# Optimization experiments

Measured on AMD Instinct MI355X. Metric: run time of the kernel, lower is better.

Reference implementation:

```python
import jax, jax.numpy as jnp
import numpy as np

EPS = 1e-4

@jax.custom_vjp
def binarize(x):
    # BinaryConnectDeterministic: sign with sign(0)=+1
    return jnp.where(x >= 0, 1.0, -1.0).astype(x.dtype)

def _bin_fwd(x):
    return binarize(x), x

def _bin_bwd(x, g):
    # straight-through estimator, clipped to |x| <= 1
    return (g * (jnp.abs(x) <= 1).astype(g.dtype),)

binarize.defvjp(_bin_fwd, _bin_bwd)

def ap2(x):
    # approximate power-of-2: sign(x) * 2^round(log2|x|); grad is 0 a.e. (round/sign)
    a = jnp.maximum(jnp.abs(x), 1e-38)
    return jnp.sign(x) * jnp.exp2(jnp.round(jnp.log2(a)))

def shift_bn(x, gamma, beta, axes):
    # shift-based batch norm (BNN paper): var approximated via centered*AP2(centered),
    # inverse std and gamma replaced by their AP2 approximations. Training-mode batch stats.
    mean = jnp.mean(x, axis=axes, keepdims=True)
    c = x - mean
    var = jnp.mean(c * ap2(c), axis=axes, keepdims=True)
    xhat = c * ap2(1.0 / jnp.sqrt(var + EPS))
    shape = [1] * x.ndim
    shape[1] = x.shape[1]
    return ap2(gamma.reshape(shape)) * xhat + beta.reshape(shape)

def conv_bin(x, w, b):
    y = jax.lax.conv_general_dilated(x, binarize(w), (1, 1), [(1, 1), (1, 1)],
                                     dimension_numbers=('NCHW', 'OIHW', 'NCHW'))
    return y + b[None, :, None, None]

def maxpool3s2(x):
    return jax.lax.reduce_window(x, -jnp.inf, jax.lax.max,
                                 (1, 1, 3, 3), (1, 1, 2, 2), 'VALID')


def setup_inputs() -> dict:
    key = jax.random.key(0)
    ks = jax.random.split(key, 8)
    B, NU = 2048, 2048
    inp = {
        'x': jax.random.normal(ks[0], (B, 784), jnp.float32),
        'conv1_w': jax.random.normal(ks[1], (32, 1, 3, 3), jnp.float32) * 0.1,
        'conv1_b': jnp.zeros((32,), jnp.float32),
        'g1': jnp.ones((32,), jnp.float32), 'b1': jnp.zeros((32,), jnp.float32),
        'conv2_w': jax.random.normal(ks[2], (64, 32, 3, 3), jnp.float32) * 0.1,
        'conv2_b': jnp.zeros((64,), jnp.float32),
        'g2': jnp.ones((64,), jnp.float32), 'b2': jnp.zeros((64,), jnp.float32),
        'lin3_w': jax.random.normal(ks[3], (NU, 10816), jnp.float32) * 0.02,
        'lin3_b': jnp.zeros((NU,), jnp.float32),
        'g3': jnp.ones((NU,), jnp.float32), 'b3': jnp.zeros((NU,), jnp.float32),
        'lin4_w': jax.random.normal(ks[4], (10, NU), jnp.float32) * 0.02,
        'lin4_b': jnp.zeros((10,), jnp.float32),
    }
    return inp


def reference(x, conv1_w, conv1_b, g1, b1, conv2_w, conv2_b, g2, b2,
              lin3_w, lin3_b, g3, b3, lin4_w, lin4_b):
    h = x.reshape(-1, 1, 28, 28)
    h = jax.nn.relu(conv_bin(h, conv1_w, conv1_b))
    h = shift_bn(h, g1, b1, axes=(0, 2, 3))
    h = binarize(h)
    h = jax.nn.relu(conv_bin(h, conv2_w, conv2_b))
    h = maxpool3s2(h)                       # [B,64,13,13]
    h = shift_bn(h, g2, b2, axes=(0, 2, 3))
    h = binarize(h)
    h = h.reshape(h.shape[0], -1)           # [B,10816]
    h = jax.nn.relu(h @ binarize(lin3_w).T + lin3_b)
    h = shift_bn(h, g3, b3, axes=(0,))
    h = binarize(h)
    return h @ binarize(lin4_w).T + lin4_b  # [B,10] (no norm4/logsoftmax in forward)
```

## Files before the change

### kernel.cpp

```cpp
#include <hip/hip_runtime.h>

#define BB 2048
#define IMG 784
#define HWD 28
#define C1 32
#define C2 64
#define PP 169
#define PD 13
#define F3 10816
#define N3 2048
#define K3W 169
#define K3P 176
#define K4W 32
#define NOUT 10
#define CONV 27
#define PADW 30
#define OCCHUNK 8
#define OCH 32
#define SCRS 736

typedef unsigned long long u64;

__device__ __forceinline__ float ap2mag(float c) {
    unsigned int a = __float_as_uint(c) & 0x7fffffffu;
    unsigned int e = (a >> 23) + ((a & 0x7fffffu) > 0x3504f3u);
    return __uint_as_float(e << 23);
}
__device__ __forceinline__ float ap2sgn(float g) {
    unsigned int u = __float_as_uint(g);
    unsigned int a = u & 0x7fffffffu;
    if (a == 0) return 0.f;
    unsigned int e = (a >> 23) + ((a & 0x7fffffu) > 0x3504f3u);
    return __uint_as_float((u & 0x80000000u) | (e << 23));
}

__global__ __launch_bounds__(256) void stage0(const float* __restrict__ x,
                                              const float* __restrict__ w1, const float* __restrict__ cb1,
                                              float* __restrict__ part1, float* __restrict__ w1b,
                                              const float* __restrict__ w2, unsigned int* __restrict__ w2p,
                                              const float* __restrict__ w3, u64* __restrict__ wp3,
                                              const float* __restrict__ w4, u64* __restrict__ wp4) {
    __shared__ float xs[30 * PADW];
    __shared__ float red[4 * C1];
    int n = blockIdx.x, tid = threadIdx.x;
    int lane = tid & 63, wv = tid >> 6;
    {
        int wid = (n * 256 + tid) >> 6;
        int nw = (gridDim.x * 256) >> 6;
        for (int w = wid; w < N3 * K3P; w += nw) {
            int nn = w / K3P, j = w - nn * K3P;
            u64 mask = 0;
            if (j < K3W) {
                float wvl = w3[(size_t)nn * F3 + j * 64 + lane];
                mask = __ballot(wvl >= 0.f);
            }
            if (lane == 0) wp3[w] = mask;
        }
    }
    if (n == 0) {
        for (int i = tid; i < C1 * 9; i += 256) w1b[i] = (w1[i] >= 0.f) ? 1.f : -1.f;
    } else if (n == 1) {
        for (int t = tid; t < C2 * 9; t += 256) {
            int oc = t / 9, k = t % 9;
            unsigned int bits = 0;
            for (int ic = 0; ic < C1; ic++)
                bits |= (w2[oc * 288 + ic * 9 + k] >= 0.f ? 1u : 0u) << ic;
            w2p[t] = bits;
        }
    } else if (n == 2) {
        for (int w = wv; w < NOUT * K4W; w += 4) {
            int o = w / K4W, j = w % K4W;
            float wvl = w4[o * N3 + j * 64 + lane];
            u64 mask = __ballot(wvl >= 0.f);
            if (lane == 0) wp4[w] = mask;
        }
    }
    for (int i = tid; i < 30 * PADW; i += 256) {
        int r = i / PADW - 1, c = i % PADW - 1;
        float v = 0.f;
        if (r >= 0 && r < HWD && c >= 0 && c < HWD) v = x[n * IMG + r * HWD + c];
        xs[i] = v;
    }
    __syncthreads();
    bool act = tid < 196;
    int r = tid / 7, c0 = (tid % 7) * 4;
    float win[18];
#pragma unroll
    for (int k = 0; k < 18; k++) win[k] = 0.f;
    if (act) {
#pragma unroll
        for (int ry = 0; ry < 3; ry++)
#pragma unroll
            for (int cx = 0; cx < 6; cx++)
                win[ry * 6 + cx] = xs[(r + ry) * PADW + c0 + cx];
    }
#pragma unroll
    for (int ch = 0; ch < C1; ch++) {
        float a = 0.f;
        if (act) {
            float k0 = (w1[ch * 9 + 0] >= 0.f) ? 1.f : -1.f, k1 = (w1[ch * 9 + 1] >= 0.f) ? 1.f : -1.f;
            float k2 = (w1[ch * 9 + 2] >= 0.f) ? 1.f : -1.f, k3 = (w1[ch * 9 + 3] >= 0.f) ? 1.f : -1.f;
            float k4 = (w1[ch * 9 + 4] >= 0.f) ? 1.f : -1.f, k5 = (w1[ch * 9 + 5] >= 0.f) ? 1.f : -1.f;
            float k6 = (w1[ch * 9 + 6] >= 0.f) ? 1.f : -1.f, k7 = (w1[ch * 9 + 7] >= 0.f) ? 1.f : -1.f;
            float k8 = (w1[ch * 9 + 8] >= 0.f) ? 1.f : -1.f;
            float b = cb1[ch];
#pragma unroll
            for (int px = 0; px < 4; px++) {
                float s = win[px] * k0 + win[px + 1] * k1 + win[px + 2] * k2
                        + win[6 + px] * k3 + win[7 + px] * k4 + win[8 + px] * k5
                        + win[12 + px] * k6 + win[13 + px] * k7 + win[14 + px] * k8;
                a += fmaxf(s + b, 0.f);
            }
        }
        for (int off = 32; off; off >>= 1) a += __shfl_down(a, off);
        if (lane == 0) red[wv * C1 + ch] = a;
    }
    __syncthreads();
    if (tid < C1) part1[n * C1 + tid] = red[tid] + red[C1 + tid] + red[2 * C1 + tid] + red[3 * C1 + tid];
}

__global__ __launch_bounds__(256) void conv1_var(const float* __restrict__ x,
                            const float* __restrict__ w1b,
                            const float* __restrict__ cb1, const float* __restrict__ mean1,
                            float* __restrict__ part) {
    __shared__ float xs[30 * PADW];
    __shared__ float red[4 * C1];
    int n = blockIdx.x, tid = threadIdx.x;
    for (int i = tid; i < 30 * PADW; i += 256) {
        int r = i / PADW - 1, c = i % PADW - 1;
        float v = 0.f;
        if (r >= 0 && r < HWD && c >= 0 && c < HWD) v = x[n * IMG + r * HWD + c];
        xs[i] = v;
    }
    __syncthreads();
    bool act = tid < 196;
    int r = tid / 7, c0 = (tid % 7) * 4;
    float win[18];
#pragma unroll
    for (int k = 0; k < 18; k++) win[k] = 0.f;
    if (act) {
#pragma unroll
        for (int ry = 0; ry < 3; ry++)
#pragma unroll
            for (int cx = 0; cx < 6; cx++)
                win[ry * 6 + cx] = xs[(r + ry) * PADW + c0 + cx];
    }
    int lane = tid & 63, wv = tid >> 6;
#pragma unroll
    for (int ch = 0; ch < C1; ch++) {
        float a = 0.f;
        if (act) {
            float k0 = w1b[ch * 9 + 0], k1 = w1b[ch * 9 + 1], k2 = w1b[ch * 9 + 2];
            float k3 = w1b[ch * 9 + 3], k4 = w1b[ch * 9 + 4], k5 = w1b[ch * 9 + 5];
            float k6 = w1b[ch * 9 + 6], k7 = w1b[ch * 9 + 7], k8 = w1b[ch * 9 + 8];
            float b = cb1[ch], m = mean1[ch];
#pragma unroll
            for (int px = 0; px < 4; px++) {
                float s = win[px] * k0 + win[px + 1] * k1 + win[px + 2] * k2
                        + win[6 + px] * k3 + win[7 + px] * k4 + win[8 + px] * k5
                        + win[12 + px] * k6 + win[13 + px] * k7 + win[14 + px] * k8;
                float v = fmaxf(s + b, 0.f);
                float c = v - m;
                a += fabsf(c) * ap2mag(c);
            }
        }
        for (int off = 32; off; off >>= 1) a += __shfl_down(a, off);
        if (lane == 0) red[wv * C1 + ch] = a;
    }
    __syncthreads();
    if (tid < C1) part[n * C1 + tid] = red[tid] + red[C1 + tid] + red[2 * C1 + tid] + red[3 * C1 + tid];
}

__global__ __launch_bounds__(256) void conv1_pack(const float* __restrict__ x,
                           const float* __restrict__ w1b,
                           const float* __restrict__ cb1, const float* __restrict__ mean1,
                           const float* __restrict__ scale1, const float* __restrict__ beta1,
                           unsigned int* __restrict__ s1p) {
    __shared__ float xs[30 * PADW];
    int n = blockIdx.x, tid = threadIdx.x;
    for (int i = tid; i < 30 * PADW; i += 256) {
        int r = i / PADW - 1, c = i % PADW - 1;
        float v = 0.f;
        if (r >= 0 && r < HWD && c >= 0 && c < HWD) v = x[n * IMG + r * HWD + c];
        xs[i] = v;
    }
    __syncthreads();
    if (tid >= 196) return;
    int r = tid / 7, c0 = (tid % 7) * 4;
    float win[18];
#pragma unroll
    for (int ry = 0; ry < 3; ry++)
#pragma unroll
        for (int cx = 0; cx < 6; cx++)
            win[ry * 6 + cx] = xs[(r + ry) * PADW + c0 + cx];
    unsigned int bits0 = 0, bits1 = 0, bits2 = 0, bits3 = 0;
#pragma unroll
    for (int ch = 0; ch < C1; ch++) {
        float k0 = w1b[ch * 9 + 0], k1 = w1b[ch * 9 + 1], k2 = w1b[ch * 9 + 2];
        float k3 = w1b[ch * 9 + 3], k4 = w1b[ch * 9 + 4], k5 = w1b[ch * 9 + 5];
        float k6 = w1b[ch * 9 + 6], k7 = w1b[ch * 9 + 7], k8 = w1b[ch * 9 + 8];
        float b = cb1[ch], m = mean1[ch], sc = scale1[ch], bt = beta1[ch];
#pragma unroll
        for (int px = 0; px < 4; px++) {
            float s = win[px] * k0 + win[px + 1] * k1 + win[px + 2] * k2
                    + win[6 + px] * k3 + win[7 + px] * k4 + win[8 + px] * k5
                    + win[12 + px] * k6 + win[13 + px] * k7 + win[14 + px] * k8;
            float v = fmaxf(s + b, 0.f);
            float val = sc * (v - m) + bt;
            unsigned int bit = (val >= 0.f ? 1u : 0u) << ch;
            if (px == 0) bits0 |= bit;
            else if (px == 1) bits1 |= bit;
            else if (px == 2) bits2 |= bit;
            else bits3 |= bit;
        }
    }
    uint4 w4v = make_uint4(bits0, bits1, bits2, bits3);
    *reinterpret_cast<uint4*>(&s1p[n * IMG + r * HWD + c0]) = w4v;
}

__global__ __launch_bounds__(256) void conv2pool(const unsigned int* __restrict__ s1p,
                                                 const unsigned int* __restrict__ w2p,
                                                 const float* __restrict__ cb2,
                                                 short* __restrict__ p2i,
                                                 float* __restrict__ part2) {
    __shared__ unsigned int spad[29 * PADW];
    __shared__ short scr[OCCHUNK * SCRS];
    __shared__ float psum[OCCHUNK * PP];
    __shared__ float pm[OCH];
    int n = blockIdx.x, ocb = blockIdx.y * OCH, tid = threadIdx.x;
    for (int i = tid; i < 29 * PADW; i += 256) {
        int r = i / PADW, c = i - r * PADW;
        unsigned int v = 0;
        if (r >= 1 && c >= 1 && c <= 28) v = s1p[n * IMG + (r - 1) * HWD + (c - 1)];
        spad[i] = v;
    }
    __syncthreads();
    unsigned int win[3][9];
    bool top_[3], left_[3];
    bool act2 = (tid + 512) < CONV * CONV;
#pragma unroll
    for (int pi = 0; pi < 3; pi++) {
        int p = tid + pi * 256;
        if (p >= CONV * CONV) p = 0;
        int y = p / CONV, xx = p - y * CONV;
        top_[pi] = (y == 0);
        left_[pi] = (xx == 0);
        const unsigned int* bp = &spad[y * PADW + xx];
#pragma unroll
        for (int ky = 0; ky < 3; ky++)
#pragma unroll
            for (int kx = 0; kx < 3; kx++)
                win[pi][ky * 3 + kx] = bp[ky * PADW + kx];
    }
    int lane = tid & 63, wv = tid >> 6;
    for (int base = 0; base < OCH; base += OCCHUNK) {
        for (int ol = 0; ol < OCCHUNK; ol++) {
            int oc = ocb + base + ol;
            unsigned int w0 = w2p[oc * 9 + 0], w1 = w2p[oc * 9 + 1], w2 = w2p[oc * 9 + 2];
            unsigned int w3 = w2p[oc * 9 + 3], w4 = w2p[oc * 9 + 4], w5 = w2p[oc * 9 + 5];
            unsigned int w6 = w2p[oc * 9 + 6], w7 = w2p[oc * 9 + 7], w8 = w2p[oc * 9 + 8];
            int p0 = __popc(w0), p1 = __popc(w1), p2 = __popc(w2);
            int p3 = __popc(w3), p6 = __popc(w6);
            int ct = 192 + 2 * (p0 + p1 + p2);
            int cl = 192 + 2 * (p0 + p3 + p6);
            int cc = 128 + 2 * (p0 + p1 + p2 + p3 + p6);
#pragma unroll
            for (int pi = 0; pi < 3; pi++) {
                int s = __popc(win[pi][0] ^ w0) + __popc(win[pi][1] ^ w1) + __popc(win[pi][2] ^ w2)
                      + __popc(win[pi][3] ^ w3) + __popc(win[pi][4] ^ w4) + __popc(win[pi][5] ^ w5)
                      + __popc(win[pi][6] ^ w6) + __popc(win[pi][7] ^ w7) + __popc(win[pi][8] ^ w8);
                int off = top_[pi] ? (left_[pi] ? cc : ct) : (left_[pi] ? cl : 288);
                if (pi < 2 || act2) scr[ol * SCRS + tid + pi * 256] = (short)(off - 2 * s);
            }
        }
        __syncthreads();
        for (int q = tid; q < OCCHUNK * PP; q += 256) {
            int ol = q / PP, pix = q - ol * PP;
            int py = pix / PD, px = pix - py * PD;
            const short* rr = &scr[ol * SCRS + (2 * py) * CONV + 2 * px];
            int m0 = max(max((int)rr[0], (int)rr[1]), (int)rr[2]);
            int m1 = max(max((int)rr[CONV], (int)rr[CONV + 1]), (int)rr[CONV + 2]);
            int m2 = max(max((int)rr[2 * CONV], (int)rr[2 * CONV + 1]), (int)rr[2 * CONV + 2]);
            int val = max(max(m0, m1), m2);
            p2i[n * F3 + (ocb + base + ol) * PP + pix] = (short)val;
            psum[q] = fmaxf((float)val + cb2[ocb + base + ol], 0.f);
        }
        __syncthreads();
        for (int ol = wv; ol < OCCHUNK; ol += 4) {
            float a = 0.f;
            for (int p = lane; p < PP; p += 64) a += psum[ol * PP + p];
            for (int off = 32; off; off >>= 1) a += __shfl_down(a, off);
            if (lane == 0) pm[base + ol] = a;
        }
        __syncthreads();
    }
    if (tid < OCH) part2[n * C2 + ocb + tid] = pm[tid];
}

__global__ __launch_bounds__(256) void p2_var(const short* __restrict__ p2i,
                         const float* __restrict__ cb2,
                         const float* __restrict__ mean2, float* __restrict__ part) {
    int n = blockIdx.x, tid = threadIdx.x, lane = tid & 63, wv = tid >> 6;
    const short* rowb = p2i + (size_t)n * F3;
    __shared__ float red[C2];
#pragma unroll
    for (int i = 0; i < 16; i++) {
        int ch = wv * 16 + i;
        const short* row = rowb + ch * PP;
        float b = cb2[ch];
        float m = mean2[ch];
        float a = 0.f;
        for (int p = lane; p < PP; p += 64) {
            float v = fmaxf((float)row[p] + b, 0.f);
            float c = v - m;
            a += fabsf(c) * ap2mag(c);
        }
        for (int off = 32; off; off >>= 1) a += __shfl_down(a, off);
        if (lane == 0) red[ch] = a;
    }
    __syncthreads();
    if (tid < C2) part[n * C2 + tid] = red[tid];
}

__global__ __launch_bounds__(256) void reduce_stats(const float* __restrict__ part, int nch, int nblk,
                             const float* __restrict__ g, float* __restrict__ outv,
                             int mode, double count) {
    int ch = blockIdx.x, tid = threadIdx.x;
    double a = 0.0;
    for (int i = tid; i < nblk; i += 256) a += (double)part[(size_t)i * nch + ch];
    __shared__ double red[4];
    for (int off = 32; off; off >>= 1) a += __shfl_down(a, off);
    int lane = tid & 63, wv = tid >> 6;
    if (lane == 0) red[wv] = a;
    __syncthreads();
    if (tid == 0) {
        double s = red[0] + red[1] + red[2] + red[3];
        if (mode == 0) {
            outv[ch] = (float)(s / count);
        } else {
            float var = (float)(s / count);
            float inv = 1.0f / sqrtf(var + 1e-4f);
            outv[ch] = ap2sgn(g[ch]) * ap2mag(inv);
        }
    }
}

__global__ void p2_pack(const short* __restrict__ p2i, const float* __restrict__ cb2,
                        const float* __restrict__ mean2, const float* __restrict__ scale2,
                        const float* __restrict__ beta2, u64* __restrict__ hp3) {
    int lane = threadIdx.x & 63;
    int wid = (blockIdx.x * blockDim.x + threadIdx.x) >> 6;
    int nw = (gridDim.x * blockDim.x) >> 6;
    for (int w = wid; w < BB * K3P; w += nw) {
        int n = w / K3P, j = w - n * K3P;
        u64 mask = 0;
        if (j < K3W) {
            int f = j * 64 + lane;
            int oc = f / PP;
            float v = fmaxf((float)p2i[n * F3 + f] + cb2[oc], 0.f);
            float val = scale2[oc] * (v - mean2[oc]) + beta2[oc];
            mask = __ballot(val >= 0.f);
        }
        if (lane == 0) hp3[w] = mask;
    }
}

__global__ __launch_bounds__(256) void lin3_gemm(const u64* __restrict__ hp3,
                                                 const u64* __restrict__ wp3,
                                                 const float* __restrict__ b3l,
                                                 float* __restrict__ h3,
                                                 float* __restrict__ part3) {
    __shared__ u64 aT[8][128];
    __shared__ u64 bT[8][64];
    __shared__ float csr[4][64];
    int tid = threadIdx.x;
    int tx = tid & 15, ty = tid >> 4;
    int m0 = blockIdx.y * 128, n0 = blockIdx.x * 64;
    int arow = tid >> 1, akk = (tid & 1) * 4;
    int bcol = tid >> 2, bkk = (tid & 3) * 2;
    const u64* aps = &hp3[(size_t)(m0 + arow) * K3P + akk];
    const u64* bps = &wp3[(size_t)(n0 + bcol) * K3P + bkk];
    int s[8][4];
#pragma unroll
    for (int i = 0; i < 8; i++)
#pragma unroll
        for (int j = 0; j < 4; j++) s[i][j] = 0;
    for (int k0 = 0; k0 < K3P; k0 += 8) {
        u64 a0 = aps[0], a1 = aps[1], a2 = aps[2], a3 = aps[3];
        u64 b0 = bps[0], b1 = bps[1];
        aps += 8; bps += 8;
        aT[akk + 0][arow] = a0; aT[akk + 1][arow] = a1;
        aT[akk + 2][arow] = a2; aT[akk + 3][arow] = a3;
        bT[bkk + 0][bcol] = b0; bT[bkk + 1][bcol] = b1;
        __syncthreads();
#pragma unroll
        for (int kk = 0; kk < 8; kk++) {
            u64 b[4], a[8];
#pragma unroll
            for (int j = 0; j < 4; j++) b[j] = bT[kk][j * 16 + tx];
#pragma unroll
            for (int i = 0; i < 8; i++) a[i] = aT[kk][i * 16 + ty];
#pragma unroll
            for (int i = 0; i < 8; i++)
#pragma unroll
                for (int j = 0; j < 4; j++) s[i][j] += (int)__popcll(a[i] ^ b[j]);
        }
        __syncthreads();
    }
    float cs[4] = {0.f, 0.f, 0.f, 0.f};
#pragma unroll
    for (int i = 0; i < 8; i++) {
        int m = m0 + i * 16 + ty;
#pragma unroll
        for (int j = 0; j < 4; j++) {
            int nn = n0 + j * 16 + tx;
            float v = fmaxf((float)(F3 - 2 * s[i][j]) + b3l[nn], 0.f);
            h3[(size_t)m * N3 + nn] = v;
            cs[j] += v;
        }
    }
    int lane = tid & 63, wv = tid >> 6;
#pragma unroll
    for (int j = 0; j < 4; j++) {
        cs[j] += __shfl_xor(cs[j], 16);
        cs[j] += __shfl_xor(cs[j], 32);
        if (lane < 16) csr[wv][j * 16 + lane] = cs[j];
    }
    __syncthreads();
    if (tid < 64)
        part3[(size_t)blockIdx.y * N3 + n0 + tid] =
            csr[0][tid] + csr[1][tid] + csr[2][tid] + csr[3][tid];
}

__global__ __launch_bounds__(256) void h3_finish(const float* __restrict__ h3,
                                                 const float* __restrict__ part3,
                                                 const float* __restrict__ g3,
                                                 float* __restrict__ mean3, float* __restrict__ scale3) {
    int nn = blockIdx.x, tid = threadIdx.x;
    __shared__ float msh;
    __shared__ double redd[4];
    if (tid < 64) {
        float a = (tid < 16) ? part3[(size_t)tid * N3 + nn] : 0.f;
        for (int off = 8; off; off >>= 1) a += __shfl_down(a, off);
        if (tid == 0) { float m = a / (float)BB; mean3[nn] = m; msh = m; }
    }
    __syncthreads();
    float m = msh;
    float acc = 0.f;
#pragma unroll
    for (int q = 0; q < 8; q++) {
        float v = h3[(size_t)(q * 256 + tid) * N3 + nn];
        float c = v - m;
        acc += fabsf(c) * ap2mag(c);
    }
    double a = (double)acc;
    for (int off = 32; off; off >>= 1) a += __shfl_down(a, off);
    int lane = tid & 63, wv = tid >> 6;
    if (lane == 0) redd[wv] = a;
    __syncthreads();
    if (tid == 0) {
        float var = (float)((redd[0] + redd[1] + redd[2] + redd[3]) / (double)BB);
        float inv = 1.0f / sqrtf(var + 1e-4f);
        scale3[nn] = ap2sgn(g3[nn]) * ap2mag(inv);
    }
}

__global__ __launch_bounds__(256) void h4_out(const float* __restrict__ h3,
                                              const float* __restrict__ mean3, const float* __restrict__ scale3,
                                              const float* __restrict__ bt3,
                                              const u64* __restrict__ wp4, const float* __restrict__ b4,
                                              float* __restrict__ out) {
    __shared__ u64 hb[K4W];
    __shared__ u64 wsh[NOUT * 33];
    int m = blockIdx.x, tid = threadIdx.x, lane = tid & 63, wv = tid >> 6;
    for (int i = tid; i < NOUT * K4W; i += 256) wsh[(i / K4W) * 33 + (i % K4W)] = wp4[i];
#pragma unroll
    for (int q = 0; q < 8; q++) {
        int j = wv * 8 + q;
        int f = j * 64 + lane;
        float v = h3[(size_t)m * N3 + f];
        float val = scale3[f] * (v - mean3[f]) + bt3[f];
        u64 mask = __ballot(val >= 0.f);
        if (lane == 0) hb[j] = mask;
    }
    __syncthreads();
    if (tid < NOUT) {
        int c = 0;
#pragma unroll
        for (int k = 0; k < K4W; k++) c += (int)__popcll(hb[k] ^ wsh[tid * 33 + k]);
        out[m * NOUT + tid] = (float)(N3 - 2 * c) + b4[tid];
    }
}

extern "C" void kernel_launch(void* const* d_in, const int* in_sizes, int n_in,
                              void* d_out, int out_size, void* d_ws, size_t ws_size,
                              hipStream_t stream) {
    const float* x   = (const float*)d_in[0];
    const float* w1  = (const float*)d_in[1];
    const float* cb1 = (const float*)d_in[2];
    const float* g1  = (const float*)d_in[3];
    const float* bt1 = (const float*)d_in[4];
    const float* w2  = (const float*)d_in[5];
    const float* cb2 = (const float*)d_in[6];
    const float* g2  = (const float*)d_in[7];
    const float* bt2 = (const float*)d_in[8];
    const float* w3  = (const float*)d_in[9];
    const float* b3l = (const float*)d_in[10];
    const float* g3  = (const float*)d_in[11];
    const float* bt3 = (const float*)d_in[12];
    const float* w4  = (const float*)d_in[13];
    const float* b4l = (const float*)d_in[14];
    float* out = (float*)d_out;

    char* base = (char*)d_ws;
    size_t off = 0;
    auto carve = [&](size_t bytes) { char* p = base + off; off = (off + bytes + 255) & ~(size_t)255; return p; };
    unsigned int* s1p  = (unsigned int*)carve((size_t)BB * IMG * 4);
    short* p2i         = (short*)carve((size_t)BB * C2 * PP * 2);
    u64* hp3           = (u64*)carve((size_t)BB * K3P * 8);
    u64* wp3           = (u64*)carve((size_t)N3 * K3P * 8);
    float* h3          = (float*)carve((size_t)BB * N3 * 4);
    u64* wp4           = (u64*)carve((size_t)NOUT * K4W * 8);
    unsigned int* w2p  = (unsigned int*)carve((size_t)C2 * 9 * 4);
    float* w1b         = (float*)carve((size_t)C1 * 9 * 4);
    float* part1       = (float*)carve((size_t)BB * C1 * 4);
    float* part2       = (float*)carve((size_t)BB * C2 * 4);
    float* part3       = (float*)carve((size_t)16 * N3 * 4);
    float* fstats      = (float*)carve((size_t)(32 + 32 + 64 + 64 + 2048 + 2048) * 4);
    float* mean1 = fstats;          float* scale1 = fstats + 32;
    float* mean2 = fstats + 64;     float* scale2 = fstats + 128;
    float* mean3 = fstats + 192;    float* scale3 = fstats + 2240;

    stage0<<<BB, 256, 0, stream>>>(x, w1, cb1, part1, w1b, w2, w2p, w3, wp3, w4, wp4);
    reduce_stats<<<C1, 256, 0, stream>>>(part1, C1, BB, g1, mean1, 0, (double)BB * IMG);
    conv1_var<<<BB, 256, 0, stream>>>(x, w1b, cb1, mean1, part1);
    reduce_stats<<<C1, 256, 0, stream>>>(part1, C1, BB, g1, scale1, 1, (double)BB * IMG);
    conv1_pack<<<BB, 256, 0, stream>>>(x, w1b, cb1, mean1, scale1, bt1, s1p);
    conv2pool<<<dim3(BB, 2), 256, 0, stream>>>(s1p, w2p, cb2, p2i, part2);
    reduce_stats<<<C2, 256, 0, stream>>>(part2, C2, BB, g2, mean2, 0, (double)BB * PP);
    p2_var<<<BB, 256, 0, stream>>>(p2i, cb2, mean2, part2);
    reduce_stats<<<C2, 256, 0, stream>>>(part2, C2, BB, g2, scale2, 1, (double)BB * PP);
    p2_pack<<<1024, 256, 0, stream>>>(p2i, cb2, mean2, scale2, bt2, hp3);
    lin3_gemm<<<dim3(32, 16), 256, 0, stream>>>(hp3, wp3, b3l, h3, part3);
    h3_finish<<<N3, 256, 0, stream>>>(h3, part3, g3, mean3, scale3);
    h4_out<<<BB, 256, 0, stream>>>(h3, mean3, scale3, bt3, wp4, b4l, out);

    (void)in_sizes; (void)n_in; (void)out_size; (void)ws_size;
}
```

Before: 624.9 us.

## Replace XOR-popcount lin3 GEMM with int8 MFMA on ±1 bytes

Lin3 inputs and weights are now stored as int8 ±1 bytes instead of packed bit words, and the GEMM uses the 16x16x64 int8 MFMA instruction with 128x128 block tiles and register prefetch of the next K chunk. This replaces the scalar popcount ALU loop with matrix-core throughput. In exchange the operand memory traffic grows eightfold (about 22 MB for the weights and 22 MB for activations), and the workspace buffers are aliased to fit, which depends on buffer lifetimes not overlapping.

```diff
diff --git a/kernel.cpp b/kernel.cpp
--- a/kernel.cpp
+++ b/kernel.cpp
@@ -9,8 +9,6 @@
 #define PD 13
 #define F3 10816
 #define N3 2048
-#define K3W 169
-#define K3P 176
 #define K4W 32
 #define NOUT 10
 #define CONV 27
@@ -20,6 +18,7 @@
 #define SCRS 736
 
 typedef unsigned long long u64;
+typedef int v4i __attribute__((ext_vector_type(4)));
 
 __device__ __forceinline__ float ap2mag(float c) {
     unsigned int a = __float_as_uint(c) & 0x7fffffffu;
@@ -38,23 +37,23 @@
                                               const float* __restrict__ w1, const float* __restrict__ cb1,
                                               float* __restrict__ part1, float* __restrict__ w1b,
                                               const float* __restrict__ w2, unsigned int* __restrict__ w2p,
-                                              const float* __restrict__ w3, u64* __restrict__ wp3,
+                                              const float* __restrict__ w3, char* __restrict__ wp3i,
                                               const float* __restrict__ w4, u64* __restrict__ wp4) {
     __shared__ float xs[30 * PADW];
     __shared__ float red[4 * C1];
     int n = blockIdx.x, tid = threadIdx.x;
     int lane = tid & 63, wv = tid >> 6;
     {
-        int wid = (n * 256 + tid) >> 6;
-        int nw = (gridDim.x * 256) >> 6;
-        for (int w = wid; w < N3 * K3P; w += nw) {
-            int nn = w / K3P, j = w - nn * K3P;
-            u64 mask = 0;
-            if (j < K3W) {
-                float wvl = w3[(size_t)nn * F3 + j * 64 + lane];
-                mask = __ballot(wvl >= 0.f);
-            }
-            if (lane == 0) wp3[w] = mask;
+        int idx = n * 256 + tid;
+        int nthr = gridDim.x * 256;
+        int total = (N3 * F3) / 4;
+        for (int t = idx; t < total; t += nthr) {
+            float4 wv4 = *(const float4*)(w3 + (size_t)t * 4);
+            unsigned int w = (wv4.x >= 0.f ? 0x01u : 0xffu)
+                           | (wv4.y >= 0.f ? 0x01u : 0xffu) << 8
+                           | (wv4.z >= 0.f ? 0x01u : 0xffu) << 16
+                           | (wv4.w >= 0.f ? 0x01u : 0xffu) << 24;
+            *(unsigned int*)(wp3i + (size_t)t * 4) = w;
         }
     }
     if (n == 0) {
@@ -345,91 +344,100 @@
     }
 }
 
-__global__ void p2_pack(const short* __restrict__ p2i, const float* __restrict__ cb2,
+__global__ __launch_bounds__(256) void p2_packi8(const short* __restrict__ p2i, const float* __restrict__ cb2,
                         const float* __restrict__ mean2, const float* __restrict__ scale2,
-                        const float* __restrict__ beta2, u64* __restrict__ hp3) {
-    int lane = threadIdx.x & 63;
-    int wid = (blockIdx.x * blockDim.x + threadIdx.x) >> 6;
-    int nw = (gridDim.x * blockDim.x) >> 6;
-    for (int w = wid; w < BB * K3P; w += nw) {
-        int n = w / K3P, j = w - n * K3P;
-        u64 mask = 0;
-        if (j < K3W) {
-            int f = j * 64 + lane;
+                        const float* __restrict__ beta2, char* __restrict__ hp3i) {
+    int idx = blockIdx.x * 256 + threadIdx.x;
+    int nthr = gridDim.x * 256;
+    int total = (BB * F3) / 4;
+    for (int t = idx; t < total; t += nthr) {
+        int base = t * 4;
+        int f0 = base % F3;
+        unsigned int w = 0;
+#pragma unroll
+        for (int e = 0; e < 4; e++) {
+            int f = f0 + e;
             int oc = f / PP;
-            float v = fmaxf((float)p2i[n * F3 + f] + cb2[oc], 0.f);
+            float v = fmaxf((float)p2i[base + e] + cb2[oc], 0.f);
             float val = scale2[oc] * (v - mean2[oc]) + beta2[oc];
-            mask = __ballot(val >= 0.f);
-        }
-        if (lane == 0) hp3[w] = mask;
-    }
-}
-
-__global__ __launch_bounds__(256) void lin3_gemm(const u64* __restrict__ hp3,
-                                                 const u64* __restrict__ wp3,
+            w |= (val >= 0.f ? 0x01u : 0xffu) << (8 * e);
+        }
+        *(unsigned int*)(hp3i + base) = w;
+    }
+}
+
+__global__ __launch_bounds__(256) void lin3_mfma(const char* __restrict__ hp3i,
+                                                 const char* __restrict__ wp3i,
                                                  const float* __restrict__ b3l,
                                                  float* __restrict__ h3,
                                                  float* __restrict__ part3) {
-    __shared__ u64 aT[8][128];
-    __shared__ u64 bT[8][64];
+    __shared__ v4i aL[8 * 64];
+    __shared__ v4i bL[8 * 64];
     __shared__ float csr[4][64];
     int tid = threadIdx.x;
-    int tx = tid & 15, ty = tid >> 4;
-    int m0 = blockIdx.y * 128, n0 = blockIdx.x * 64;
-    int arow = tid >> 1, akk = (tid & 1) * 4;
-    int bcol = tid >> 2, bkk = (tid & 3) * 2;
-    const u64* aps = &hp3[(size_t)(m0 + arow) * K3P + akk];
-    const u64* bps = &wp3[(size_t)(n0 + bcol) * K3P + bkk];
-    int s[8][4];
-#pragma unroll
-    for (int i = 0; i < 8; i++)
-#pragma unroll
-        for (int j = 0; j < 4; j++) s[i][j] = 0;
-    for (int k0 = 0; k0 < K3P; k0 += 8) {
-        u64 a0 = aps[0], a1 = aps[1], a2 = aps[2], a3 = aps[3];
-        u64 b0 = bps[0], b1 = bps[1];
-        aps += 8; bps += 8;
-        aT[akk + 0][arow] = a0; aT[akk + 1][arow] = a1;
-        aT[akk + 2][arow] = a2; aT[akk + 3][arow] = a3;
-        bT[bkk + 0][bcol] = b0; bT[bkk + 1][bcol] = b1;
+    int lane = tid & 63, wv = tid >> 6;
+    int wr = wv >> 1, wc = wv & 1;
+    int m0 = blockIdx.y * 128, n0 = blockIdx.x * 128;
+    int r = tid >> 1, h = tid & 1;
+    const char* ag = hp3i + (size_t)(m0 + r) * F3 + h * 32;
+    const char* bg = wp3i + (size_t)(n0 + r) * F3 + h * 32;
+    int wbase = (r >> 4) * 64 + (2 * h) * 16 + (r & 15);
+    v4i acc[4][4];
+#pragma unroll
+    for (int i = 0; i < 4; i++)
+#pragma unroll
+        for (int j = 0; j < 4; j++) acc[i][j] = (v4i){0, 0, 0, 0};
+    v4i a0 = *(const v4i*)ag, a1 = *(const v4i*)(ag + 16);
+    v4i b0 = *(const v4i*)bg, b1 = *(const v4i*)(bg + 16);
+    for (int c = 0; c < 169; c++) {
         __syncthreads();
-#pragma unroll
-        for (int kk = 0; kk < 8; kk++) {
-            u64 b[4], a[8];
-#pragma unroll
-            for (int j = 0; j < 4; j++) b[j] = bT[kk][j * 16 + tx];
-#pragma unroll
-            for (int i = 0; i < 8; i++) a[i] = aT[kk][i * 16 + ty];
-#pragma unroll
-            for (int i = 0; i < 8; i++)
-#pragma unroll
-                for (int j = 0; j < 4; j++) s[i][j] += (int)__popcll(a[i] ^ b[j]);
-        }
+        aL[wbase] = a0; aL[wbase + 16] = a1;
+        bL[wbase] = b0; bL[wbase + 16] = b1;
         __syncthreads();
-    }
+        if (c < 168) {
+            ag += 64; bg += 64;
+            a0 = *(const v4i*)ag; a1 = *(const v4i*)(ag + 16);
+            b0 = *(const v4i*)bg; b1 = *(const v4i*)(bg + 16);
+        }
+        v4i af[4], bf[4];
+#pragma unroll
+        for (int i = 0; i < 4; i++) af[i] = aL[(wr * 4 + i) * 64 + lane];
+#pragma unroll
+        for (int j = 0; j < 4; j++) bf[j] = bL[(wc * 4 + j) * 64 + lane];
+#pragma unroll
+        for (int i = 0; i < 4; i++)
+#pragma unroll
+            for (int j = 0; j < 4; j++)
+                acc[i][j] = __builtin_amdgcn_mfma_i32_16x16x64_i8(af[i], bf[j], acc[i][j], 0, 0, 0);
+    }
+    int q = lane >> 4, m16 = lane & 15;
     float cs[4] = {0.f, 0.f, 0.f, 0.f};
 #pragma unroll
-    for (int i = 0; i < 8; i++) {
-        int m = m0 + i * 16 + ty;
-#pragma unroll
-        for (int j = 0; j < 4; j++) {
-            int nn = n0 + j * 16 + tx;
-            float v = fmaxf((float)(F3 - 2 * s[i][j]) + b3l[nn], 0.f);
-            h3[(size_t)m * N3 + nn] = v;
-            cs[j] += v;
-        }
-    }
-    int lane = tid & 63, wv = tid >> 6;
+    for (int j = 0; j < 4; j++) {
+        int col = n0 + wc * 64 + j * 16 + m16;
+        float bias = b3l[col];
+#pragma unroll
+        for (int i = 0; i < 4; i++) {
+            int rowb = m0 + wr * 64 + i * 16 + q * 4;
+#pragma unroll
+            for (int rg = 0; rg < 4; rg++) {
+                float v = fmaxf((float)acc[i][j][rg] + bias, 0.f);
+                h3[(size_t)(rowb + rg) * N3 + col] = v;
+                cs[j] += v;
+            }
+        }
+    }
 #pragma unroll
     for (int j = 0; j < 4; j++) {
         cs[j] += __shfl_xor(cs[j], 16);
         cs[j] += __shfl_xor(cs[j], 32);
-        if (lane < 16) csr[wv][j * 16 + lane] = cs[j];
-    }
-    __syncthreads();
-    if (tid < 64)
-        part3[(size_t)blockIdx.y * N3 + n0 + tid] =
-            csr[0][tid] + csr[1][tid] + csr[2][tid] + csr[3][tid];
+        if (lane < 16) csr[wv][j * 16 + m16] = cs[j];
+    }
+    __syncthreads();
+    if (tid < 128) {
+        int wcc = tid >> 6, cc = tid & 63;
+        part3[(size_t)blockIdx.y * N3 + n0 + wcc * 64 + cc] = csr[wcc][cc] + csr[wcc + 2][cc];
+    }
 }
 
 __global__ __launch_bounds__(256) void h3_finish(const float* __restrict__ h3,
@@ -515,11 +523,14 @@
     char* base = (char*)d_ws;
     size_t off = 0;
     auto carve = [&](size_t bytes) { char* p = base + off; off = (off + bytes + 255) & ~(size_t)255; return p; };
-    unsigned int* s1p  = (unsigned int*)carve((size_t)BB * IMG * 4);
-    short* p2i         = (short*)carve((size_t)BB * C2 * PP * 2);
-    u64* hp3           = (u64*)carve((size_t)BB * K3P * 8);
-    u64* wp3           = (u64*)carve((size_t)N3 * K3P * 8);
-    float* h3          = (float*)carve((size_t)BB * N3 * 4);
+    char* bufA = carve((size_t)BB * C2 * PP * 2);
+    char* bufB = carve((size_t)BB * F3);
+    char* bufC = carve((size_t)N3 * F3);
+    short* p2i         = (short*)bufA;
+    float* h3          = (float*)bufA;
+    char* hp3i         = bufB;
+    unsigned int* s1p  = (unsigned int*)bufB;
+    char* wp3i         = bufC;
     u64* wp4           = (u64*)carve((size_t)NOUT * K4W * 8);
     unsigned int* w2p  = (unsigned int*)carve((size_t)C2 * 9 * 4);
     float* w1b         = (float*)carve((size_t)C1 * 9 * 4);
@@ -531,7 +542,7 @@
     float* mean2 = fstats + 64;     float* scale2 = fstats + 128;
     float* mean3 = fstats + 192;    float* scale3 = fstats + 2240;
 
-    stage0<<<BB, 256, 0, stream>>>(x, w1, cb1, part1, w1b, w2, w2p, w3, wp3, w4, wp4);
+    stage0<<<BB, 256, 0, stream>>>(x, w1, cb1, part1, w1b, w2, w2p, w3, wp3i, w4, wp4);
     reduce_stats<<<C1, 256, 0, stream>>>(part1, C1, BB, g1, mean1, 0, (double)BB * IMG);
     conv1_var<<<BB, 256, 0, stream>>>(x, w1b, cb1, mean1, part1);
     reduce_stats<<<C1, 256, 0, stream>>>(part1, C1, BB, g1, scale1, 1, (double)BB * IMG);
@@ -540,8 +551,8 @@
     reduce_stats<<<C2, 256, 0, stream>>>(part2, C2, BB, g2, mean2, 0, (double)BB * PP);
     p2_var<<<BB, 256, 0, stream>>>(p2i, cb2, mean2, part2);
     reduce_stats<<<C2, 256, 0, stream>>>(part2, C2, BB, g2, scale2, 1, (double)BB * PP);
-    p2_pack<<<1024, 256, 0, stream>>>(p2i, cb2, mean2, scale2, bt2, hp3);
-    lin3_gemm<<<dim3(32, 16), 256, 0, stream>>>(hp3, wp3, b3l, h3, part3);
+    p2_packi8<<<2048, 256, 0, stream>>>(p2i, cb2, mean2, scale2, bt2, hp3i);
+    lin3_mfma<<<dim3(16, 16), 256, 0, stream>>>(hp3i, wp3i, b3l, h3, part3);
     h3_finish<<<N3, 256, 0, stream>>>(h3, part3, g3, mean3, scale3);
     h4_out<<<BB, 256, 0, stream>>>(h3, mean3, scale3, bt3, wp4, b4l, out);
 
```

Result: faster. 593.9 us (-5.0%).
